# Kernel tuning notes

Hardware: AMD Instinct MI355X
Metric: run time of the kernel (lower is better)

The kernel has to match this reference:

```python
import jax, jax.numpy as jnp
import numpy as np

B = 8192          # batch_size
NB = 4096         # num_banks (== mask length)
PAD = NB // 2     # reflect pad on each side


def setup_inputs() -> dict:
    key = jax.random.key(0)
    k1, k2, k3 = jax.random.split(key, 3)
    logits = jax.random.normal(k1, (NB,), dtype=jnp.float32) * 0.1
    u = jax.random.uniform(k2, (B, NB), dtype=jnp.float32)          # Bernoulli uniforms
    shift = jax.random.randint(k3, (B,), 0, NB, dtype=jnp.int32)    # per-sample shift
    return {"logits": logits, "u": u, "shift": shift}


def reference(logits, u, shift):
    # Bernoulli(sigmoid(logits)) sample via inverse-CDF on externally supplied uniforms
    p = jax.nn.sigmoid(logits)                       # (NB,)
    grid = (u < p).astype(jnp.float32)               # (B, NB)
    # Bernoulli log_prob summed over banks: g*log(p) + (1-g)*log(1-p)
    log_probs = (grid * jax.nn.log_sigmoid(logits)
                 + (1.0 - grid) * jax.nn.log_sigmoid(-logits)).sum(axis=1)  # (B,)
    # reflect-pad along bank axis, then gather a shifted window of length NB
    padded = jnp.pad(grid, ((0, 0), (PAD, PAD)), mode="reflect")    # (B, NB+2*PAD)
    idx = shift[:, None].astype(jnp.int32) + jnp.arange(NB, dtype=jnp.int32)[None, :]
    masks = jnp.take_along_axis(padded, idx, axis=1)[:, None, :]    # (B, 1, NB)
    return masks, log_probs
```

## Files before the change

### kernel.cpp

```cpp
#include <hip/hip_runtime.h>
#include <math.h>

#define NB 4096
#define PAD 2048
#define TPB 1024
#define WPB 16

typedef float f32x4 __attribute__((ext_vector_type(4)));

__device__ __forceinline__ int mirror_idx(int i) {
    i = ::abs(i);
    return (i < NB) ? i : (2 * (NB - 1) - i);
}

__global__ void fbmp_precompute(const float* __restrict__ logits, float* __restrict__ ws) {
    int j = blockIdx.x * blockDim.x + threadIdx.x;
    if (j >= NB) return;
    float x = logits[j];
    double xd = (double)x;
    float e = (float)exp(-xd);
    float p = 1.0f / (1.0f + e);
    float lsp = (float)(-log1p(exp(-xd)));
    float lsn = (float)(-log1p(exp(xd)));
    ws[j] = p;
    ws[NB + j] = lsp;
    ws[2 * NB + j] = lsn;
}

__global__ __launch_bounds__(TPB, 4) void fbmp_wave(
    const float* __restrict__ u, const int* __restrict__ shift,
    const float* __restrict__ ws,
    float* __restrict__ masks, float* __restrict__ logp, int B)
{
    __shared__ float tbl[3 * NB];
    __shared__ unsigned long long words[WPB][64];

    const int t = threadIdx.x;

    {
        const float4* __restrict__ src = (const float4*)ws;
        float4* __restrict__ dst = (float4*)tbl;
        #pragma unroll
        for (int c = 0; c < (3 * NB / 4) / TPB; ++c)
            dst[t + c * TPB] = src[t + c * TPB];
    }
    __syncthreads();

    const int lane = t & 63;
    const int wid  = t >> 6;
    const int row  = blockIdx.x * WPB + wid;
    if (row >= B) return;

    const int s = shift[row] - PAD;
    const float4* __restrict__ u4   = (const float4*)(u + (size_t)row * NB);
    const float4* __restrict__ p4   = (const float4*)tbl;
    const float4* __restrict__ lsp4 = (const float4*)(tbl + NB);
    const float4* __restrict__ lsn4 = (const float4*)(tbl + 2 * NB);

    float accw[4] = {0.0f, 0.0f, 0.0f, 0.0f};
    unsigned long long myword = 0ull;

    #pragma unroll
    for (int c = 0; c < 16; ++c) {
        const int i = lane + 64 * c;
        float4 uv = u4[i];
        float4 pv = p4[i];
        float4 ap = lsp4[i];
        float4 an = lsn4[i];
        bool c0 = uv.x < pv.x;
        bool c1 = uv.y < pv.y;
        bool c2 = uv.z < pv.z;
        bool c3 = uv.w < pv.w;
        accw[c & 3] += (c0 ? ap.x : an.x) + (c1 ? ap.y : an.y)
                     + (c2 ? ap.z : an.z) + (c3 ? ap.w : an.w);
        unsigned long long b0 = __ballot(c0);
        unsigned long long b1 = __ballot(c1);
        unsigned long long b2 = __ballot(c2);
        unsigned long long b3 = __ballot(c3);
        if ((lane >> 2) == c) {
            unsigned long long m0 = (lane & 1) ? b1 : b0;
            unsigned long long m1 = (lane & 1) ? b3 : b2;
            myword = (lane & 2) ? m1 : m0;
        }
    }
    words[wid][lane] = myword;

    #pragma unroll
    for (int w = 0; w < 4; ++w) {
        #pragma unroll
        for (int off = 32; off > 0; off >>= 1)
            accw[w] += __shfl_down(accw[w], off, 64);
    }
    if (lane == 0) {
        float tt = 0.0f;
        tt += accw[0];
        tt += accw[1];
        tt += accw[2];
        tt += accw[3];
        logp[row] = tt;
    }

    const unsigned int* __restrict__ w32 = (const unsigned int*)&words[wid][0];
    float* __restrict__ mrow = masks + (size_t)row * NB;
    #pragma unroll
    for (int c = 0; c < 16; ++c) {
        const int i = lane + 64 * c;
        const int k = 4 * i + s;
        f32x4 o;
        {
            const int j = mirror_idx(k + 0);
            const int w64 = ((j >> 8) << 2) | (j & 3);
            const int bit = (j >> 2) & 63;
            o.x = ((w32[(w64 << 1) | (bit >> 5)] >> (bit & 31)) & 1u) ? 1.0f : 0.0f;
        }
        {
            const int j = mirror_idx(k + 1);
            const int w64 = ((j >> 8) << 2) | (j & 3);
            const int bit = (j >> 2) & 63;
            o.y = ((w32[(w64 << 1) | (bit >> 5)] >> (bit & 31)) & 1u) ? 1.0f : 0.0f;
        }
        {
            const int j = mirror_idx(k + 2);
            const int w64 = ((j >> 8) << 2) | (j & 3);
            const int bit = (j >> 2) & 63;
            o.z = ((w32[(w64 << 1) | (bit >> 5)] >> (bit & 31)) & 1u) ? 1.0f : 0.0f;
        }
        {
            const int j = mirror_idx(k + 3);
            const int w64 = ((j >> 8) << 2) | (j & 3);
            const int bit = (j >> 2) & 63;
            o.w = ((w32[(w64 << 1) | (bit >> 5)] >> (bit & 31)) & 1u) ? 1.0f : 0.0f;
        }
        __builtin_nontemporal_store(o, (f32x4*)mrow + i);
    }
}

extern "C" void kernel_launch(void* const* d_in, const int* in_sizes, int n_in,
                              void* d_out, int out_size, void* d_ws, size_t ws_size,
                              hipStream_t stream) {
    const float* logits = (const float*)d_in[0];
    const float* u      = (const float*)d_in[1];
    const int*   shift  = (const int*)d_in[2];
    const int B = in_sizes[2];

    float* ws    = (float*)d_ws;
    float* masks = (float*)d_out;
    float* logp  = (float*)d_out + (size_t)B * NB;

    fbmp_precompute<<<(NB + 255) / 256, 256, 0, stream>>>(logits, ws);
    const int grid = (B + WPB - 1) / WPB;
    fbmp_wave<<<grid, TPB, 0, stream>>>(u, shift, ws, masks, logp, B);
}
```

Baseline: 249.9 us.

## Split wave kernel into bit-pack and mask-expand kernels via workspace

Splits the single fused kernel into two. The first computes Bernoulli bits and log-probs, reading the probability tables directly from global memory instead of staging them in LDS, and issues all u loads up front. It writes the packed bits to a workspace buffer. The second kernel expands those bits into shifted, reflected masks with a small LDS footprint, so more blocks can be resident. A plain fused fallback kernel runs when the workspace is too small. The split adds one extra launch and a small round trip of packed bits through global memory.

After: 242.1 us. 1.03x faster.

```diff
diff --git a/kernel.cpp b/kernel.cpp
--- a/kernel.cpp
+++ b/kernel.cpp
@@ -3,8 +3,6 @@
 
 #define NB 4096
 #define PAD 2048
-#define TPB 1024
-#define WPB 16
 
 typedef float f32x4 __attribute__((ext_vector_type(4)));
 
@@ -27,35 +25,24 @@
     ws[2 * NB + j] = lsn;
 }
 
-__global__ __launch_bounds__(TPB, 4) void fbmp_wave(
-    const float* __restrict__ u, const int* __restrict__ shift,
-    const float* __restrict__ ws,
-    float* __restrict__ masks, float* __restrict__ logp, int B)
+__global__ __launch_bounds__(256, 4) void fbmp_bits(
+    const float* __restrict__ u, const float* __restrict__ ws,
+    unsigned long long* __restrict__ pb, float* __restrict__ logp, int B)
 {
-    __shared__ float tbl[3 * NB];
-    __shared__ unsigned long long words[WPB][64];
-
     const int t = threadIdx.x;
-
-    {
-        const float4* __restrict__ src = (const float4*)ws;
-        float4* __restrict__ dst = (float4*)tbl;
-        #pragma unroll
-        for (int c = 0; c < (3 * NB / 4) / TPB; ++c)
-            dst[t + c * TPB] = src[t + c * TPB];
-    }
-    __syncthreads();
-
     const int lane = t & 63;
     const int wid  = t >> 6;
-    const int row  = blockIdx.x * WPB + wid;
+    const int row  = blockIdx.x * 4 + wid;
     if (row >= B) return;
 
-    const int s = shift[row] - PAD;
     const float4* __restrict__ u4   = (const float4*)(u + (size_t)row * NB);
-    const float4* __restrict__ p4   = (const float4*)tbl;
-    const float4* __restrict__ lsp4 = (const float4*)(tbl + NB);
-    const float4* __restrict__ lsn4 = (const float4*)(tbl + 2 * NB);
+    const float4* __restrict__ p4   = (const float4*)(ws);
+    const float4* __restrict__ lsp4 = (const float4*)(ws + NB);
+    const float4* __restrict__ lsn4 = (const float4*)(ws + 2 * NB);
+
+    float4 uvv[16];
+    #pragma unroll
+    for (int c = 0; c < 16; ++c) uvv[c] = u4[lane + 64 * c];
 
     float accw[4] = {0.0f, 0.0f, 0.0f, 0.0f};
     unsigned long long myword = 0ull;
@@ -63,14 +50,13 @@
     #pragma unroll
     for (int c = 0; c < 16; ++c) {
         const int i = lane + 64 * c;
-        float4 uv = u4[i];
         float4 pv = p4[i];
         float4 ap = lsp4[i];
         float4 an = lsn4[i];
-        bool c0 = uv.x < pv.x;
-        bool c1 = uv.y < pv.y;
-        bool c2 = uv.z < pv.z;
-        bool c3 = uv.w < pv.w;
+        bool c0 = uvv[c].x < pv.x;
+        bool c1 = uvv[c].y < pv.y;
+        bool c2 = uvv[c].z < pv.z;
+        bool c3 = uvv[c].w < pv.w;
         accw[c & 3] += (c0 ? ap.x : an.x) + (c1 ? ap.y : an.y)
                      + (c2 ? ap.z : an.z) + (c3 ? ap.w : an.w);
         unsigned long long b0 = __ballot(c0);
@@ -83,7 +69,8 @@
             myword = (lane & 2) ? m1 : m0;
         }
     }
-    words[wid][lane] = myword;
+
+    pb[(size_t)row * 64 + lane] = myword;
 
     #pragma unroll
     for (int w = 0; w < 4; ++w) {
@@ -99,9 +86,26 @@
         tt += accw[3];
         logp[row] = tt;
     }
+}
+
+__global__ __launch_bounds__(256, 8) void fbmp_masks(
+    const unsigned long long* __restrict__ pb, const int* __restrict__ shift,
+    float* __restrict__ masks, int B)
+{
+    __shared__ unsigned long long words[4][64];
+
+    const int t = threadIdx.x;
+    const int lane = t & 63;
+    const int wid  = t >> 6;
+    const int row  = blockIdx.x * 4 + wid;
+    if (row >= B) return;
+
+    words[wid][lane] = pb[(size_t)row * 64 + lane];
+    const int s = shift[row] - PAD;
 
     const unsigned int* __restrict__ w32 = (const unsigned int*)&words[wid][0];
     float* __restrict__ mrow = masks + (size_t)row * NB;
+
     #pragma unroll
     for (int c = 0; c < 16; ++c) {
         const int i = lane + 64 * c;
@@ -132,6 +136,65 @@
             o.w = ((w32[(w64 << 1) | (bit >> 5)] >> (bit & 31)) & 1u) ? 1.0f : 0.0f;
         }
         __builtin_nontemporal_store(o, (f32x4*)mrow + i);
+    }
+}
+
+__global__ __launch_bounds__(256) void fbmp_fused(
+    const float* __restrict__ u, const int* __restrict__ shift,
+    const float* __restrict__ ws,
+    float* __restrict__ masks, float* __restrict__ logp)
+{
+    __shared__ float sg[NB];
+    __shared__ float sred[4];
+
+    const int b = blockIdx.x;
+    const float4* __restrict__ u4   = (const float4*)(u + (size_t)b * NB);
+    const float4* __restrict__ p4   = (const float4*)(ws);
+    const float4* __restrict__ lsp4 = (const float4*)(ws + NB);
+    const float4* __restrict__ lsn4 = (const float4*)(ws + 2 * NB);
+
+    float acc = 0.0f;
+    for (int i = threadIdx.x; i < NB / 4; i += 256) {
+        float4 uv = u4[i];
+        float4 pv = p4[i];
+        float4 ap = lsp4[i];
+        float4 an = lsn4[i];
+        bool c0 = uv.x < pv.x;
+        bool c1 = uv.y < pv.y;
+        bool c2 = uv.z < pv.z;
+        bool c3 = uv.w < pv.w;
+        acc += (c0 ? ap.x : an.x) + (c1 ? ap.y : an.y)
+             + (c2 ? ap.z : an.z) + (c3 ? ap.w : an.w);
+        float4 g;
+        g.x = c0 ? 1.0f : 0.0f;
+        g.y = c1 ? 1.0f : 0.0f;
+        g.z = c2 ? 1.0f : 0.0f;
+        g.w = c3 ? 1.0f : 0.0f;
+        ((float4*)sg)[i] = g;
+    }
+    #pragma unroll
+    for (int off = 32; off > 0; off >>= 1)
+        acc += __shfl_down(acc, off, 64);
+    const int lane = threadIdx.x & 63;
+    const int wid  = threadIdx.x >> 6;
+    if (lane == 0) sred[wid] = acc;
+    __syncthreads();
+    if (threadIdx.x == 0) {
+        float t = 0.0f;
+        #pragma unroll
+        for (int w = 0; w < 4; ++w) t += sred[w];
+        logp[b] = t;
+    }
+    const int s = shift[b] - PAD;
+    float4* __restrict__ m4 = (float4*)(masks + (size_t)b * NB);
+    for (int i = threadIdx.x; i < NB / 4; i += 256) {
+        int k = 4 * i + s;
+        float4 o;
+        o.x = sg[mirror_idx(k + 0)];
+        o.y = sg[mirror_idx(k + 1)];
+        o.z = sg[mirror_idx(k + 2)];
+        o.w = sg[mirror_idx(k + 3)];
+        m4[i] = o;
     }
 }
 
@@ -148,6 +211,15 @@
     float* logp  = (float*)d_out + (size_t)B * NB;
 
     fbmp_precompute<<<(NB + 255) / 256, 256, 0, stream>>>(logits, ws);
-    const int grid = (B + WPB - 1) / WPB;
-    fbmp_wave<<<grid, TPB, 0, stream>>>(u, shift, ws, masks, logp, B);
-}
+
+    const size_t tbl_bytes = (size_t)3 * NB * sizeof(float);
+    const size_t pb_bytes  = (size_t)B * 64 * sizeof(unsigned long long);
+    if (ws_size >= tbl_bytes + pb_bytes) {
+        unsigned long long* pb = (unsigned long long*)((char*)d_ws + tbl_bytes);
+        const int grid = (B + 3) / 4;
+        fbmp_bits <<<grid, 256, 0, stream>>>(u, ws, pb, logp, B);
+        fbmp_masks<<<grid, 256, 0, stream>>>(pb, shift, masks, B);
+    } else {
+        fbmp_fused<<<B, 256, 0, stream>>>(u, shift, ws, masks, logp);
+    }
+}
```

## Split waves into producer and consumer roles with double-buffered bit masks

Applied to the files above, without the earlier changes.

Reworks the main kernel into a warp-specialized pipeline. Four producer waves load u rows, compute the Bernoulli bits and log-probs, and write packed bits to a double-buffered shared array. Four consumer waves write the reflected, shifted mask rows for the previous set, so loads of the next rows overlap the stores of the current ones. In exchange, each block loads the table once for 16 rows but uses half the threads and adds a block-wide barrier per stage. Only half the waves touch memory at any given time.

Result: slower. 261.2 us (+4.5%).

```diff
diff --git a/kernel.cpp b/kernel.cpp
--- a/kernel.cpp
+++ b/kernel.cpp
@@ -3,8 +3,9 @@
 
 #define NB 4096
 #define PAD 2048
-#define TPB 1024
-#define WPB 16
+#define TPB 512
+#define PW 4
+#define KSETS 4
 
 typedef float f32x4 __attribute__((ext_vector_type(4)));
 
@@ -27,13 +28,13 @@
     ws[2 * NB + j] = lsn;
 }
 
-__global__ __launch_bounds__(TPB, 4) void fbmp_wave(
+__global__ __launch_bounds__(TPB, 4) void fbmp_pc(
     const float* __restrict__ u, const int* __restrict__ shift,
     const float* __restrict__ ws,
     float* __restrict__ masks, float* __restrict__ logp, int B)
 {
     __shared__ float tbl[3 * NB];
-    __shared__ unsigned long long words[WPB][64];
+    __shared__ unsigned long long bits[2][PW][64];
 
     const int t = threadIdx.x;
 
@@ -44,94 +45,120 @@
         for (int c = 0; c < (3 * NB / 4) / TPB; ++c)
             dst[t + c * TPB] = src[t + c * TPB];
     }
+
+    const int lane = t & 63;
+    const int wv   = t >> 6;
+    const bool producer = (wv < PW);
+    const int role = producer ? wv : (wv - PW);
+    const int b0 = blockIdx.x * (PW * KSETS);
+
+    int sh[KSETS];
+    if (!producer) {
+        #pragma unroll
+        for (int s = 0; s < KSETS; ++s) {
+            const int row = b0 + s * PW + role;
+            sh[s] = (row < B) ? (shift[row] - PAD) : 0;
+        }
+    }
     __syncthreads();
 
-    const int lane = t & 63;
-    const int wid  = t >> 6;
-    const int row  = blockIdx.x * WPB + wid;
-    if (row >= B) return;
-
-    const int s = shift[row] - PAD;
-    const float4* __restrict__ u4   = (const float4*)(u + (size_t)row * NB);
     const float4* __restrict__ p4   = (const float4*)tbl;
     const float4* __restrict__ lsp4 = (const float4*)(tbl + NB);
     const float4* __restrict__ lsn4 = (const float4*)(tbl + 2 * NB);
 
-    float accw[4] = {0.0f, 0.0f, 0.0f, 0.0f};
-    unsigned long long myword = 0ull;
+    for (int s = 0; s <= KSETS; ++s) {
+        if (producer && s < KSETS) {
+            const int row = b0 + s * PW + role;
+            if (row < B) {
+                const float4* __restrict__ u4 = (const float4*)(u + (size_t)row * NB);
+                float4 uvv[16];
+                #pragma unroll
+                for (int c = 0; c < 16; ++c) uvv[c] = u4[lane + 64 * c];
 
-    #pragma unroll
-    for (int c = 0; c < 16; ++c) {
-        const int i = lane + 64 * c;
-        float4 uv = u4[i];
-        float4 pv = p4[i];
-        float4 ap = lsp4[i];
-        float4 an = lsn4[i];
-        bool c0 = uv.x < pv.x;
-        bool c1 = uv.y < pv.y;
-        bool c2 = uv.z < pv.z;
-        bool c3 = uv.w < pv.w;
-        accw[c & 3] += (c0 ? ap.x : an.x) + (c1 ? ap.y : an.y)
-                     + (c2 ? ap.z : an.z) + (c3 ? ap.w : an.w);
-        unsigned long long b0 = __ballot(c0);
-        unsigned long long b1 = __ballot(c1);
-        unsigned long long b2 = __ballot(c2);
-        unsigned long long b3 = __ballot(c3);
-        if ((lane >> 2) == c) {
-            unsigned long long m0 = (lane & 1) ? b1 : b0;
-            unsigned long long m1 = (lane & 1) ? b3 : b2;
-            myword = (lane & 2) ? m1 : m0;
+                float accw[4] = {0.0f, 0.0f, 0.0f, 0.0f};
+                unsigned long long myword = 0ull;
+                #pragma unroll
+                for (int c = 0; c < 16; ++c) {
+                    const int i = lane + 64 * c;
+                    float4 pv = p4[i];
+                    float4 ap = lsp4[i];
+                    float4 an = lsn4[i];
+                    bool c0 = uvv[c].x < pv.x;
+                    bool c1 = uvv[c].y < pv.y;
+                    bool c2 = uvv[c].z < pv.z;
+                    bool c3 = uvv[c].w < pv.w;
+                    accw[c & 3] += (c0 ? ap.x : an.x) + (c1 ? ap.y : an.y)
+                                 + (c2 ? ap.z : an.z) + (c3 ? ap.w : an.w);
+                    unsigned long long b0w = __ballot(c0);
+                    unsigned long long b1w = __ballot(c1);
+                    unsigned long long b2w = __ballot(c2);
+                    unsigned long long b3w = __ballot(c3);
+                    if ((lane >> 2) == c) {
+                        unsigned long long m0 = (lane & 1) ? b1w : b0w;
+                        unsigned long long m1 = (lane & 1) ? b3w : b2w;
+                        myword = (lane & 2) ? m1 : m0;
+                    }
+                }
+                bits[s & 1][role][lane] = myword;
+
+                #pragma unroll
+                for (int w = 0; w < 4; ++w) {
+                    #pragma unroll
+                    for (int off = 32; off > 0; off >>= 1)
+                        accw[w] += __shfl_down(accw[w], off, 64);
+                }
+                if (lane == 0) {
+                    float tt = 0.0f;
+                    tt += accw[0];
+                    tt += accw[1];
+                    tt += accw[2];
+                    tt += accw[3];
+                    logp[row] = tt;
+                }
+            }
         }
-    }
-    words[wid][lane] = myword;
-
-    #pragma unroll
-    for (int w = 0; w < 4; ++w) {
-        #pragma unroll
-        for (int off = 32; off > 0; off >>= 1)
-            accw[w] += __shfl_down(accw[w], off, 64);
-    }
-    if (lane == 0) {
-        float tt = 0.0f;
-        tt += accw[0];
-        tt += accw[1];
-        tt += accw[2];
-        tt += accw[3];
-        logp[row] = tt;
-    }
-
-    const unsigned int* __restrict__ w32 = (const unsigned int*)&words[wid][0];
-    float* __restrict__ mrow = masks + (size_t)row * NB;
-    #pragma unroll
-    for (int c = 0; c < 16; ++c) {
-        const int i = lane + 64 * c;
-        const int k = 4 * i + s;
-        f32x4 o;
-        {
-            const int j = mirror_idx(k + 0);
-            const int w64 = ((j >> 8) << 2) | (j & 3);
-            const int bit = (j >> 2) & 63;
-            o.x = ((w32[(w64 << 1) | (bit >> 5)] >> (bit & 31)) & 1u) ? 1.0f : 0.0f;
+        if (!producer && s >= 1) {
+            const int ss = s - 1;
+            const int row = b0 + ss * PW + role;
+            if (row < B) {
+                const unsigned int* __restrict__ w32 =
+                    (const unsigned int*)&bits[ss & 1][role][0];
+                float* __restrict__ mrow = masks + (size_t)row * NB;
+                const int sshift = sh[ss];
+                #pragma unroll
+                for (int c = 0; c < 16; ++c) {
+                    const int i = lane + 64 * c;
+                    const int k = 4 * i + sshift;
+                    f32x4 o;
+                    {
+                        const int j = mirror_idx(k + 0);
+                        const int w64 = ((j >> 8) << 2) | (j & 3);
+                        const int bit = (j >> 2) & 63;
+                        o.x = ((w32[(w64 << 1) | (bit >> 5)] >> (bit & 31)) & 1u) ? 1.0f : 0.0f;
+                    }
+                    {
+                        const int j = mirror_idx(k + 1);
+                        const int w64 = ((j >> 8) << 2) | (j & 3);
+                        const int bit = (j >> 2) & 63;
+                        o.y = ((w32[(w64 << 1) | (bit >> 5)] >> (bit & 31)) & 1u) ? 1.0f : 0.0f;
+                    }
+                    {
+                        const int j = mirror_idx(k + 2);
+                        const int w64 = ((j >> 8) << 2) | (j & 3);
+                        const int bit = (j >> 2) & 63;
+                        o.z = ((w32[(w64 << 1) | (bit >> 5)] >> (bit & 31)) & 1u) ? 1.0f : 0.0f;
+                    }
+                    {
+                        const int j = mirror_idx(k + 3);
+                        const int w64 = ((j >> 8) << 2) | (j & 3);
+                        const int bit = (j >> 2) & 63;
+                        o.w = ((w32[(w64 << 1) | (bit >> 5)] >> (bit & 31)) & 1u) ? 1.0f : 0.0f;
+                    }
+                    __builtin_nontemporal_store(o, (f32x4*)mrow + i);
+                }
+            }
         }
-        {
-            const int j = mirror_idx(k + 1);
-            const int w64 = ((j >> 8) << 2) | (j & 3);
-            const int bit = (j >> 2) & 63;
-            o.y = ((w32[(w64 << 1) | (bit >> 5)] >> (bit & 31)) & 1u) ? 1.0f : 0.0f;
-        }
-        {
-            const int j = mirror_idx(k + 2);
-            const int w64 = ((j >> 8) << 2) | (j & 3);
-            const int bit = (j >> 2) & 63;
-            o.z = ((w32[(w64 << 1) | (bit >> 5)] >> (bit & 31)) & 1u) ? 1.0f : 0.0f;
-        }
-        {
-            const int j = mirror_idx(k + 3);
-            const int w64 = ((j >> 8) << 2) | (j & 3);
-            const int bit = (j >> 2) & 63;
-            o.w = ((w32[(w64 << 1) | (bit >> 5)] >> (bit & 31)) & 1u) ? 1.0f : 0.0f;
-        }
-        __builtin_nontemporal_store(o, (f32x4*)mrow + i);
+        __syncthreads();
     }
 }
 
@@ -148,6 +175,8 @@
     float* logp  = (float*)d_out + (size_t)B * NB;
 
     fbmp_precompute<<<(NB + 255) / 256, 256, 0, stream>>>(logits, ws);
-    const int grid = (B + WPB - 1) / WPB;
-    fbmp_wave<<<grid, TPB, 0, stream>>>(u, shift, ws, masks, logp, B);
+
+    const int rows_per_block = PW * KSETS;
+    const int grid = (B + rows_per_block - 1) / rows_per_block;
+    fbmp_pc<<<grid, TPB, 0, stream>>>(u, shift, ws, masks, logp, B);
 }
```
